# Performance work log

Hardware: AMD Instinct MI355X
Metric: run time of the kernel (lower is better)

The kernel has to match this reference:

```python
import jax, jax.numpy as jnp
import numpy as np

NUM_EXPERTS = 16
TOP_K = 2
HIDDEN = 2048
INTER = 1408
TOKENS = 4096


def setup_inputs() -> dict:
    key = jax.random.key(0)
    k0, k1, k2, k3, k4 = jax.random.split(key, 5)
    scale = 0.02
    return {
        "hidden_states": jax.random.normal(k0, (TOKENS, HIDDEN), jnp.float32),
        "router_logits": jax.random.normal(k1, (TOKENS, NUM_EXPERTS), jnp.float32),
        # SwiGLU expert weights, stacked over the expert dim.
        "w_gate": jax.random.normal(k2, (NUM_EXPERTS, HIDDEN, INTER), jnp.float32) * scale,
        "w_up": jax.random.normal(k3, (NUM_EXPERTS, HIDDEN, INTER), jnp.float32) * scale,
        "w_down": jax.random.normal(k4, (NUM_EXPERTS, INTER, HIDDEN), jnp.float32) * scale,
    }


def reference(hidden_states, router_logits, w_gate, w_up, w_down):
    # Routing (router_use_softmax=False branch): topk on raw logits,
    # then softmax over the selected top-k logits.
    topk_weights, topk_ids = jax.lax.top_k(router_logits, TOP_K)  # [T,K]
    topk_weights = jax.nn.softmax(topk_weights, axis=-1)

    T = hidden_states.shape[0]
    # Dense combine matrix [T, E]: weight of expert e for token t (0 if not selected).
    combine = jnp.zeros((T, NUM_EXPERTS), hidden_states.dtype)
    combine = combine.at[jnp.arange(T)[:, None], topk_ids].add(topk_weights)

    # Expert SwiGLU FFNs, computed densely over all tokens per expert and
    # masked/weighted by the combine matrix (same math as gather->FFN->scatter).
    g = jnp.einsum("th,ehi->eti", hidden_states, w_gate)  # [E,T,I]
    u = jnp.einsum("th,ehi->eti", hidden_states, w_up)    # [E,T,I]
    a = jax.nn.silu(g) * u                                  # [E,T,I]
    y = jnp.einsum("eti,eih->eth", a, w_down)             # [E,T,H]

    # Weighted scatter-combine: sum_e combine[t,e] * y[e,t,:]
    return jnp.einsum("eth,te->th", y, combine)            # [T,H]
```

## Files before the change

kernel.cpp:

```cpp
#include <hip/hip_runtime.h>
#include <hip/hip_bf16.h>
#include <cstdint>

#define NTOK 4096
#define NEXP 16
#define HID 2048
#define INTER 1408
#define BK 32
#define LDA 40
#define MAXTILES 80

typedef __attribute__((ext_vector_type(8))) short bf16x8;
typedef __attribute__((ext_vector_type(4))) float f32x4;


__device__ inline unsigned pack_bf16(float lo, float hi) {
  unsigned a = __builtin_bit_cast(unsigned, lo) + 0x8000u;
  unsigned b = __builtin_bit_cast(unsigned, hi) + 0x8000u;
  return __builtin_amdgcn_perm(b, a, 0x07060302u);
}

__global__ void k_router(const float* __restrict__ logits, int* __restrict__ topk_id,
                         float* __restrict__ topk_w, int* __restrict__ counts) {
  int t = blockIdx.x * blockDim.x + threadIdx.x;
  if (t >= NTOK) return;
  const float* l = logits + (size_t)t * NEXP;
  float b0 = -1e30f, b1 = -1e30f; int i0 = 0, i1 = 0;
#pragma unroll
  for (int i = 0; i < NEXP; i++) {
    float v = l[i];
    if (v > b0) { b1 = b0; i1 = i0; b0 = v; i0 = i; }
    else if (v > b1) { b1 = v; i1 = i; }
  }
  float e = __expf(b1 - b0);
  float inv = 1.f / (1.f + e);
  topk_id[t * 2] = i0; topk_id[t * 2 + 1] = i1;
  topk_w[t * 2] = inv; topk_w[t * 2 + 1] = e * inv;
  atomicAdd(&counts[i0], 1);
  atomicAdd(&counts[i1], 1);
}

__global__ void k_build(int* __restrict__ ws_i) {
  if (threadIdx.x == 0) {
    int off = 0, nt = 0;
    for (int e = 0; e < NEXP; e++) {
      int c = ws_i[e];
      ws_i[32 + e] = off;
      int tiles = (c + 127) >> 7;
      for (int mt = 0; mt < tiles; mt++) { ws_i[64 + nt] = e; ws_i[144 + nt] = mt; nt++; }
      off += c;
    }
    ws_i[48] = nt;
  }
}

__global__ void k_scatter(const int* __restrict__ topk_id, const float* __restrict__ topk_w,
                          int* __restrict__ ws_i, int* __restrict__ list_tok,
                          float* __restrict__ list_w) {
  int t = blockIdx.x * blockDim.x + threadIdx.x;
  if (t >= NTOK) return;
#pragma unroll
  for (int k = 0; k < 2; k++) {
    int e = topk_id[t * 2 + k];
    int slot = ws_i[32 + e] + atomicAdd(&ws_i[16 + e], 1);
    list_tok[slot] = t;
    list_w[slot] = topk_w[t * 2 + k];
  }
}

__global__ __launch_bounds__(256, 2) void k_gateup(
    const float* __restrict__ hidden, const float* __restrict__ w_gate,
    const float* __restrict__ w_up, const int* __restrict__ ws_i,
    const int* __restrict__ list_tok, __hip_bfloat16* __restrict__ act) {
  __shared__ unsigned short sA[128 * LDA];
  __shared__ unsigned short sBg[64 * LDA];
  __shared__ unsigned short sBu[64 * LDA];
  __shared__ int sTok[128];

  int tileId = blockIdx.y;
  if (tileId >= ws_i[48]) return;
  int e = ws_i[64 + tileId];
  int mt = ws_i[144 + tileId];
  int c = ws_i[e];
  int offE = ws_i[32 + e];
  int m0 = mt * 128;
  int n0 = blockIdx.x * 64;
  int tid = threadIdx.x;

  if (tid < 128) {
    int r = m0 + tid;
    int rr = r < c ? r : c - 1;
    sTok[tid] = list_tok[offE + rr];
  }
  __syncthreads();

  const float* wg = w_gate + (size_t)e * HID * INTER + n0;
  const float* wu = w_up + (size_t)e * HID * INTER + n0;

  int lane = tid & 63;
  int wave = tid >> 6;
  int wm = wave & 1, wn = wave >> 1;

  f32x4 accG[4][2], accU[4][2];
#pragma unroll
  for (int i = 0; i < 4; i++)
#pragma unroll
    for (int j = 0; j < 2; j++) { accG[i][j] = (f32x4)(0.f); accU[i][j] = (f32x4)(0.f); }

  int ar = tid >> 1;
  int ah = (tid & 1) * 16;
  const float* aSrc = hidden + (size_t)sTok[ar] * HID + ah;

  int bn = tid & 63;
  int bkg = tid >> 6;
  const float* bgSrc = wg + bn + (size_t)(bkg * 8) * INTER;
  const float* buSrc = wu + bn + (size_t)(bkg * 8) * INTER;

  int kq = (lane >> 4) * 8;
  int ml = lane & 15;

  for (int k0 = 0; k0 < HID; k0 += BK) {
    const float4* ap = (const float4*)(aSrc + k0);
    float4 a0 = ap[0], a1 = ap[1], a2 = ap[2], a3 = ap[3];
    float g[8], u[8];
    const float* bg = bgSrc + (size_t)k0 * INTER;
    const float* bu = buSrc + (size_t)k0 * INTER;
#pragma unroll
    for (int j = 0; j < 8; j++) { g[j] = bg[(size_t)j * INTER]; u[j] = bu[(size_t)j * INTER]; }

    __syncthreads();
    {
      uint4 w0 = make_uint4(pack_bf16(a0.x, a0.y), pack_bf16(a0.z, a0.w),
                            pack_bf16(a1.x, a1.y), pack_bf16(a1.z, a1.w));
      uint4 w1 = make_uint4(pack_bf16(a2.x, a2.y), pack_bf16(a2.z, a2.w),
                            pack_bf16(a3.x, a3.y), pack_bf16(a3.z, a3.w));
      *(uint4*)&sA[ar * LDA + ah] = w0;
      *(uint4*)&sA[ar * LDA + ah + 8] = w1;
      *(uint4*)&sBg[bn * LDA + bkg * 8] = make_uint4(
          pack_bf16(g[0], g[1]), pack_bf16(g[2], g[3]),
          pack_bf16(g[4], g[5]), pack_bf16(g[6], g[7]));
      *(uint4*)&sBu[bn * LDA + bkg * 8] = make_uint4(
          pack_bf16(u[0], u[1]), pack_bf16(u[2], u[3]),
          pack_bf16(u[4], u[5]), pack_bf16(u[6], u[7]));
    }
    __syncthreads();

    bf16x8 af[4], bgf[2], buf2[2];
#pragma unroll
    for (int ni = 0; ni < 2; ni++) {
      bgf[ni] = *(const bf16x8*)&sBg[(wn * 32 + ni * 16 + ml) * LDA + kq];
      buf2[ni] = *(const bf16x8*)&sBu[(wn * 32 + ni * 16 + ml) * LDA + kq];
    }
#pragma unroll
    for (int mi = 0; mi < 4; mi++)
      af[mi] = *(const bf16x8*)&sA[(wm * 64 + mi * 16 + ml) * LDA + kq];
#pragma unroll
    for (int mi = 0; mi < 4; mi++)
#pragma unroll
      for (int ni = 0; ni < 2; ni++) {
        accG[mi][ni] = __builtin_amdgcn_mfma_f32_16x16x32_bf16(af[mi], bgf[ni], accG[mi][ni], 0, 0, 0);
        accU[mi][ni] = __builtin_amdgcn_mfma_f32_16x16x32_bf16(af[mi], buf2[ni], accU[mi][ni], 0, 0, 0);
      }
  }

  int rq = (lane >> 4) * 4;
#pragma unroll
  for (int mi = 0; mi < 4; mi++)
#pragma unroll
    for (int r = 0; r < 4; r++) {
      int mrow = wm * 64 + mi * 16 + rq + r;
      int mglob = m0 + mrow;
      if (mglob < c) {
        size_t arow = (size_t)(offE + mglob);
#pragma unroll
        for (int ni = 0; ni < 2; ni++) {
          float gv = accG[mi][ni][r], uv = accU[mi][ni][r];
          float av = gv / (1.f + __expf(-gv)) * uv;
          int ncol = n0 + wn * 32 + ni * 16 + ml;
          act[arow * INTER + ncol] = __float2bfloat16(av);
        }
      }
    }
}

__global__ __launch_bounds__(256, 2) void k_down(
    const __hip_bfloat16* __restrict__ act, const float* __restrict__ w_down,
    const int* __restrict__ ws_i, const int* __restrict__ list_tok,
    const float* __restrict__ list_w, float* __restrict__ out) {
  __shared__ unsigned short sA[128 * LDA];
  __shared__ unsigned short sB[128 * LDA];
  __shared__ int sTok[128];
  __shared__ float sW[128];

  int tileId = blockIdx.y;
  if (tileId >= ws_i[48]) return;
  int e = ws_i[64 + tileId];
  int mt = ws_i[144 + tileId];
  int c = ws_i[e];
  int offE = ws_i[32 + e];
  int m0 = mt * 128;
  int n0 = blockIdx.x * 128;
  int tid = threadIdx.x;

  if (tid < 128) {
    int r = m0 + tid;
    int rr = r < c ? r : c - 1;
    sTok[tid] = list_tok[offE + rr];
    sW[tid] = list_w[offE + rr];
  }
  __syncthreads();

  int lane = tid & 63;
  int wave = tid >> 6;
  int wm = wave & 1, wn = wave >> 1;
  f32x4 acc[4][4];
#pragma unroll
  for (int i = 0; i < 4; i++)
#pragma unroll
    for (int j = 0; j < 4; j++) acc[i][j] = (f32x4)(0.f);

  int ar = tid >> 1;
  int ah = (tid & 1) * 16;
  const __hip_bfloat16* aRow;
  {
    int r = m0 + ar;
    int rr = r < c ? r : c - 1;
    aRow = act + (size_t)(offE + rr) * INTER + ah;
  }
  int bn = tid & 127;
  int bkg2 = tid >> 7;
  const float* bSrc = w_down + (size_t)e * INTER * HID + n0 + bn;

  int kq = (lane >> 4) * 8;
  int ml = lane & 15;

  for (int k0 = 0; k0 < INTER; k0 += BK) {
    const uint4* ap = (const uint4*)(aRow + k0);
    uint4 av0 = ap[0], av1 = ap[1];
    float b[2][8];
#pragma unroll
    for (int tsk = 0; tsk < 2; tsk++) {
      const float* bp = bSrc + (size_t)(k0 + (bkg2 * 2 + tsk) * 8) * HID;
#pragma unroll
      for (int j = 0; j < 8; j++) b[tsk][j] = bp[(size_t)j * HID];
    }

    __syncthreads();
    *(uint4*)&sA[ar * LDA + ah] = av0;
    *(uint4*)&sA[ar * LDA + ah + 8] = av1;
#pragma unroll
    for (int tsk = 0; tsk < 2; tsk++) {
      int kg = bkg2 * 2 + tsk;
      *(uint4*)&sB[bn * LDA + kg * 8] = make_uint4(
          pack_bf16(b[tsk][0], b[tsk][1]), pack_bf16(b[tsk][2], b[tsk][3]),
          pack_bf16(b[tsk][4], b[tsk][5]), pack_bf16(b[tsk][6], b[tsk][7]));
    }
    __syncthreads();

    bf16x8 af[4], bf[4];
#pragma unroll
    for (int mi = 0; mi < 4; mi++)
      af[mi] = *(const bf16x8*)&sA[(wm * 64 + mi * 16 + ml) * LDA + kq];
#pragma unroll
    for (int ni = 0; ni < 4; ni++)
      bf[ni] = *(const bf16x8*)&sB[(wn * 64 + ni * 16 + ml) * LDA + kq];
#pragma unroll
    for (int mi = 0; mi < 4; mi++)
#pragma unroll
      for (int ni = 0; ni < 4; ni++)
        acc[mi][ni] = __builtin_amdgcn_mfma_f32_16x16x32_bf16(af[mi], bf[ni], acc[mi][ni], 0, 0, 0);
  }

  int rq = (lane >> 4) * 4;
#pragma unroll
  for (int mi = 0; mi < 4; mi++)
#pragma unroll
    for (int r = 0; r < 4; r++) {
      int mrow = wm * 64 + mi * 16 + rq + r;
      if (m0 + mrow < c) {
        int t = sTok[mrow];
        float w = sW[mrow];
        float* op = out + (size_t)t * HID + n0 + wn * 64 + ml;
#pragma unroll
        for (int ni = 0; ni < 4; ni++)
          atomicAdd(op + ni * 16, w * acc[mi][ni][r]);
      }
    }
}

extern "C" void kernel_launch(void* const* d_in, const int* in_sizes, int n_in,
                              void* d_out, int out_size, void* d_ws, size_t ws_size,
                              hipStream_t stream) {
  const float* hidden = (const float*)d_in[0];
  const float* logits = (const float*)d_in[1];
  const float* w_gate = (const float*)d_in[2];
  const float* w_up = (const float*)d_in[3];
  const float* w_down = (const float*)d_in[4];
  float* out = (float*)d_out;

  int* ws_i = (int*)d_ws;
  int* topk_id = ws_i + 256;
  float* topk_w = (float*)(ws_i + 8448);
  int* list_tok = ws_i + 16640;
  float* list_w = (float*)(ws_i + 24832);
  __hip_bfloat16* act = (__hip_bfloat16*)((char*)d_ws + 33024 * 4);

  hipMemsetAsync(d_ws, 0, 256 * 4, stream);
  hipMemsetAsync(d_out, 0, (size_t)out_size * sizeof(float), stream);

  k_router<<<NTOK / 256, 256, 0, stream>>>(logits, topk_id, topk_w, ws_i);
  k_build<<<1, 64, 0, stream>>>(ws_i);
  k_scatter<<<NTOK / 256, 256, 0, stream>>>(topk_id, topk_w, ws_i, list_tok, list_w);
  k_gateup<<<dim3(INTER / 64, MAXTILES), 256, 0, stream>>>(hidden, w_gate, w_up, ws_i, list_tok, act);
  k_down<<<dim3(HID / 128, MAXTILES), 256, 0, stream>>>(act, w_down, ws_i, list_tok, list_w, out);
}
```

Before: 904.4 us.

## Pre-gather bf16 activations, prefetch tiles, and replace atomic scatter with combine kernel

Result: faster. 849.4 us (-6.1%).

```diff
diff --git a/kernel.cpp b/kernel.cpp
--- a/kernel.cpp
+++ b/kernel.cpp
@@ -56,7 +56,7 @@
 
 __global__ void k_scatter(const int* __restrict__ topk_id, const float* __restrict__ topk_w,
                           int* __restrict__ ws_i, int* __restrict__ list_tok,
-                          float* __restrict__ list_w) {
+                          float* __restrict__ list_w, int* __restrict__ slot_of) {
   int t = blockIdx.x * blockDim.x + threadIdx.x;
   if (t >= NTOK) return;
 #pragma unroll
@@ -65,17 +65,29 @@
     int slot = ws_i[32 + e] + atomicAdd(&ws_i[16 + e], 1);
     list_tok[slot] = t;
     list_w[slot] = topk_w[t * 2 + k];
-  }
-}
-
-__global__ __launch_bounds__(256, 2) void k_gateup(
-    const float* __restrict__ hidden, const float* __restrict__ w_gate,
+    slot_of[t * 2 + k] = slot;
+  }
+}
+
+__global__ __launch_bounds__(256) void k_gather(const float* __restrict__ hidden,
+                                                const int* __restrict__ list_tok,
+                                                unsigned short* __restrict__ Ab) {
+  int s = blockIdx.x, tx = threadIdx.x;
+  int t = list_tok[s];
+  const float4* src = (const float4*)(hidden + (size_t)t * HID) + tx * 2;
+  float4 a = src[0], b = src[1];
+  uint4 w = make_uint4(pack_bf16(a.x, a.y), pack_bf16(a.z, a.w),
+                       pack_bf16(b.x, b.y), pack_bf16(b.z, b.w));
+  ((uint4*)(Ab + (size_t)s * HID))[tx] = w;
+}
+
+__global__ __launch_bounds__(256, 4) void k_gateup(
+    const unsigned short* __restrict__ Ab, const float* __restrict__ w_gate,
     const float* __restrict__ w_up, const int* __restrict__ ws_i,
-    const int* __restrict__ list_tok, __hip_bfloat16* __restrict__ act) {
+    __hip_bfloat16* __restrict__ act) {
   __shared__ unsigned short sA[128 * LDA];
   __shared__ unsigned short sBg[64 * LDA];
   __shared__ unsigned short sBu[64 * LDA];
-  __shared__ int sTok[128];
 
   int tileId = blockIdx.y;
   if (tileId >= ws_i[48]) return;
@@ -87,63 +99,57 @@
   int n0 = blockIdx.x * 64;
   int tid = threadIdx.x;
 
-  if (tid < 128) {
-    int r = m0 + tid;
-    int rr = r < c ? r : c - 1;
-    sTok[tid] = list_tok[offE + rr];
-  }
-  __syncthreads();
-
-  const float* wg = w_gate + (size_t)e * HID * INTER + n0;
-  const float* wu = w_up + (size_t)e * HID * INTER + n0;
-
   int lane = tid & 63;
   int wave = tid >> 6;
   int wm = wave & 1, wn = wave >> 1;
 
-  f32x4 accG[4][2], accU[4][2];
-#pragma unroll
-  for (int i = 0; i < 4; i++)
-#pragma unroll
-    for (int j = 0; j < 2; j++) { accG[i][j] = (f32x4)(0.f); accU[i][j] = (f32x4)(0.f); }
-
   int ar = tid >> 1;
   int ah = (tid & 1) * 16;
-  const float* aSrc = hidden + (size_t)sTok[ar] * HID + ah;
+  int rA = m0 + ar; int rrA = rA < c ? rA : c - 1;
+  const unsigned short* aSrc = Ab + (size_t)(offE + rrA) * HID + ah;
 
   int bn = tid & 63;
   int bkg = tid >> 6;
-  const float* bgSrc = wg + bn + (size_t)(bkg * 8) * INTER;
-  const float* buSrc = wu + bn + (size_t)(bkg * 8) * INTER;
+  const float* bgSrc = w_gate + (size_t)e * HID * INTER + n0 + bn + (size_t)(bkg * 8) * INTER;
+  const float* buSrc = w_up   + (size_t)e * HID * INTER + n0 + bn + (size_t)(bkg * 8) * INTER;
+
+  f32x4 accG[4][2], accU[4][2];
+#pragma unroll
+  for (int i = 0; i < 4; i++)
+#pragma unroll
+    for (int j = 0; j < 2; j++) { accG[i][j] = (f32x4)(0.f); accU[i][j] = (f32x4)(0.f); }
 
   int kq = (lane >> 4) * 8;
   int ml = lane & 15;
 
+  uint4 a0r, a1r; float g[8], u[8];
+  {
+    const uint4* ap = (const uint4*)aSrc;
+    a0r = ap[0]; a1r = ap[1];
+#pragma unroll
+    for (int j = 0; j < 8; j++) { g[j] = bgSrc[(size_t)j * INTER]; u[j] = buSrc[(size_t)j * INTER]; }
+  }
+
   for (int k0 = 0; k0 < HID; k0 += BK) {
-    const float4* ap = (const float4*)(aSrc + k0);
-    float4 a0 = ap[0], a1 = ap[1], a2 = ap[2], a3 = ap[3];
-    float g[8], u[8];
-    const float* bg = bgSrc + (size_t)k0 * INTER;
-    const float* bu = buSrc + (size_t)k0 * INTER;
-#pragma unroll
-    for (int j = 0; j < 8; j++) { g[j] = bg[(size_t)j * INTER]; u[j] = bu[(size_t)j * INTER]; }
-
     __syncthreads();
-    {
-      uint4 w0 = make_uint4(pack_bf16(a0.x, a0.y), pack_bf16(a0.z, a0.w),
-                            pack_bf16(a1.x, a1.y), pack_bf16(a1.z, a1.w));
-      uint4 w1 = make_uint4(pack_bf16(a2.x, a2.y), pack_bf16(a2.z, a2.w),
-                            pack_bf16(a3.x, a3.y), pack_bf16(a3.z, a3.w));
-      *(uint4*)&sA[ar * LDA + ah] = w0;
-      *(uint4*)&sA[ar * LDA + ah + 8] = w1;
-      *(uint4*)&sBg[bn * LDA + bkg * 8] = make_uint4(
-          pack_bf16(g[0], g[1]), pack_bf16(g[2], g[3]),
-          pack_bf16(g[4], g[5]), pack_bf16(g[6], g[7]));
-      *(uint4*)&sBu[bn * LDA + bkg * 8] = make_uint4(
-          pack_bf16(u[0], u[1]), pack_bf16(u[2], u[3]),
-          pack_bf16(u[4], u[5]), pack_bf16(u[6], u[7]));
-    }
+    *(uint4*)&sA[ar * LDA + ah] = a0r;
+    *(uint4*)&sA[ar * LDA + ah + 8] = a1r;
+    *(uint4*)&sBg[bn * LDA + bkg * 8] = make_uint4(
+        pack_bf16(g[0], g[1]), pack_bf16(g[2], g[3]),
+        pack_bf16(g[4], g[5]), pack_bf16(g[6], g[7]));
+    *(uint4*)&sBu[bn * LDA + bkg * 8] = make_uint4(
+        pack_bf16(u[0], u[1]), pack_bf16(u[2], u[3]),
+        pack_bf16(u[4], u[5]), pack_bf16(u[6], u[7]));
     __syncthreads();
+
+    if (k0 + BK < HID) {
+      const uint4* ap = (const uint4*)(aSrc + k0 + BK);
+      a0r = ap[0]; a1r = ap[1];
+      const float* bg = bgSrc + (size_t)(k0 + BK) * INTER;
+      const float* bu = buSrc + (size_t)(k0 + BK) * INTER;
+#pragma unroll
+      for (int j = 0; j < 8; j++) { g[j] = bg[(size_t)j * INTER]; u[j] = bu[(size_t)j * INTER]; }
+    }
 
     bf16x8 af[4], bgf[2], buf2[2];
 #pragma unroll
@@ -183,13 +189,12 @@
     }
 }
 
-__global__ __launch_bounds__(256, 2) void k_down(
+__global__ __launch_bounds__(256, 4) void k_down(
     const __hip_bfloat16* __restrict__ act, const float* __restrict__ w_down,
-    const int* __restrict__ ws_i, const int* __restrict__ list_tok,
-    const float* __restrict__ list_w, float* __restrict__ out) {
+    const int* __restrict__ ws_i, const float* __restrict__ list_w,
+    unsigned short* __restrict__ y) {
   __shared__ unsigned short sA[128 * LDA];
-  __shared__ unsigned short sB[128 * LDA];
-  __shared__ int sTok[128];
+  __shared__ unsigned short sB[64 * LDA];
   __shared__ float sW[128];
 
   int tileId = blockIdx.y;
@@ -199,75 +204,72 @@
   int c = ws_i[e];
   int offE = ws_i[32 + e];
   int m0 = mt * 128;
-  int n0 = blockIdx.x * 128;
+  int n0 = blockIdx.x * 64;
   int tid = threadIdx.x;
 
   if (tid < 128) {
     int r = m0 + tid;
     int rr = r < c ? r : c - 1;
-    sTok[tid] = list_tok[offE + rr];
     sW[tid] = list_w[offE + rr];
   }
-  __syncthreads();
 
   int lane = tid & 63;
   int wave = tid >> 6;
   int wm = wave & 1, wn = wave >> 1;
-  f32x4 acc[4][4];
+  f32x4 acc[4][2];
 #pragma unroll
   for (int i = 0; i < 4; i++)
 #pragma unroll
-    for (int j = 0; j < 4; j++) acc[i][j] = (f32x4)(0.f);
+    for (int j = 0; j < 2; j++) acc[i][j] = (f32x4)(0.f);
 
   int ar = tid >> 1;
   int ah = (tid & 1) * 16;
-  const __hip_bfloat16* aRow;
-  {
-    int r = m0 + ar;
-    int rr = r < c ? r : c - 1;
-    aRow = act + (size_t)(offE + rr) * INTER + ah;
-  }
-  int bn = tid & 127;
-  int bkg2 = tid >> 7;
-  const float* bSrc = w_down + (size_t)e * INTER * HID + n0 + bn;
+  int rA = m0 + ar; int rrA = rA < c ? rA : c - 1;
+  const unsigned short* aSrc = (const unsigned short*)act + (size_t)(offE + rrA) * INTER + ah;
+
+  int bn = tid & 63;
+  int bkg = tid >> 6;
+  const float* bSrc = w_down + (size_t)e * INTER * HID + (size_t)(bkg * 8) * HID + n0 + bn;
 
   int kq = (lane >> 4) * 8;
   int ml = lane & 15;
 
+  uint4 a0r, a1r; float b[8];
+  {
+    const uint4* ap = (const uint4*)aSrc;
+    a0r = ap[0]; a1r = ap[1];
+#pragma unroll
+    for (int j = 0; j < 8; j++) b[j] = bSrc[(size_t)j * HID];
+  }
+
   for (int k0 = 0; k0 < INTER; k0 += BK) {
-    const uint4* ap = (const uint4*)(aRow + k0);
-    uint4 av0 = ap[0], av1 = ap[1];
-    float b[2][8];
-#pragma unroll
-    for (int tsk = 0; tsk < 2; tsk++) {
-      const float* bp = bSrc + (size_t)(k0 + (bkg2 * 2 + tsk) * 8) * HID;
-#pragma unroll
-      for (int j = 0; j < 8; j++) b[tsk][j] = bp[(size_t)j * HID];
-    }
-
     __syncthreads();
-    *(uint4*)&sA[ar * LDA + ah] = av0;
-    *(uint4*)&sA[ar * LDA + ah + 8] = av1;
-#pragma unroll
-    for (int tsk = 0; tsk < 2; tsk++) {
-      int kg = bkg2 * 2 + tsk;
-      *(uint4*)&sB[bn * LDA + kg * 8] = make_uint4(
-          pack_bf16(b[tsk][0], b[tsk][1]), pack_bf16(b[tsk][2], b[tsk][3]),
-          pack_bf16(b[tsk][4], b[tsk][5]), pack_bf16(b[tsk][6], b[tsk][7]));
-    }
+    *(uint4*)&sA[ar * LDA + ah] = a0r;
+    *(uint4*)&sA[ar * LDA + ah + 8] = a1r;
+    *(uint4*)&sB[bn * LDA + bkg * 8] = make_uint4(
+        pack_bf16(b[0], b[1]), pack_bf16(b[2], b[3]),
+        pack_bf16(b[4], b[5]), pack_bf16(b[6], b[7]));
     __syncthreads();
 
-    bf16x8 af[4], bf[4];
+    if (k0 + BK < INTER) {
+      const uint4* ap = (const uint4*)(aSrc + k0 + BK);
+      a0r = ap[0]; a1r = ap[1];
+      const float* bp = bSrc + (size_t)(k0 + BK) * HID;
+#pragma unroll
+      for (int j = 0; j < 8; j++) b[j] = bp[(size_t)j * HID];
+    }
+
+    bf16x8 af[4], bf[2];
+#pragma unroll
+    for (int ni = 0; ni < 2; ni++)
+      bf[ni] = *(const bf16x8*)&sB[(wn * 32 + ni * 16 + ml) * LDA + kq];
 #pragma unroll
     for (int mi = 0; mi < 4; mi++)
       af[mi] = *(const bf16x8*)&sA[(wm * 64 + mi * 16 + ml) * LDA + kq];
 #pragma unroll
-    for (int ni = 0; ni < 4; ni++)
-      bf[ni] = *(const bf16x8*)&sB[(wn * 64 + ni * 16 + ml) * LDA + kq];
-#pragma unroll
     for (int mi = 0; mi < 4; mi++)
 #pragma unroll
-      for (int ni = 0; ni < 4; ni++)
+      for (int ni = 0; ni < 2; ni++)
         acc[mi][ni] = __builtin_amdgcn_mfma_f32_16x16x32_bf16(af[mi], bf[ni], acc[mi][ni], 0, 0, 0);
   }
 
@@ -278,14 +280,39 @@
     for (int r = 0; r < 4; r++) {
       int mrow = wm * 64 + mi * 16 + rq + r;
       if (m0 + mrow < c) {
-        int t = sTok[mrow];
         float w = sW[mrow];
-        float* op = out + (size_t)t * HID + n0 + wn * 64 + ml;
-#pragma unroll
-        for (int ni = 0; ni < 4; ni++)
-          atomicAdd(op + ni * 16, w * acc[mi][ni][r]);
+        size_t yrow = (size_t)(offE + m0 + mrow);
+#pragma unroll
+        for (int ni = 0; ni < 2; ni++) {
+          int ncol = n0 + wn * 32 + ni * 16 + ml;
+          float v = w * acc[mi][ni][r];
+          y[yrow * HID + ncol] = (unsigned short)(pack_bf16(v, 0.f) & 0xffffu);
+        }
       }
     }
+}
+
+__global__ __launch_bounds__(256) void k_combine(const unsigned short* __restrict__ y,
+                                                 const int* __restrict__ slot_of,
+                                                 float* __restrict__ out) {
+  int t = blockIdx.x, tx = threadIdx.x;
+  size_t s0 = (size_t)slot_of[t * 2], s1 = (size_t)slot_of[t * 2 + 1];
+  uint4 v0 = ((const uint4*)(y + s0 * HID))[tx];
+  uint4 v1 = ((const uint4*)(y + s1 * HID))[tx];
+  float r[8];
+  unsigned p0[4] = {v0.x, v0.y, v0.z, v0.w};
+  unsigned p1[4] = {v1.x, v1.y, v1.z, v1.w};
+#pragma unroll
+  for (int i = 0; i < 4; i++) {
+    float lo0 = __builtin_bit_cast(float, p0[i] << 16);
+    float hi0 = __builtin_bit_cast(float, p0[i] & 0xffff0000u);
+    float lo1 = __builtin_bit_cast(float, p1[i] << 16);
+    float hi1 = __builtin_bit_cast(float, p1[i] & 0xffff0000u);
+    r[i * 2] = lo0 + lo1; r[i * 2 + 1] = hi0 + hi1;
+  }
+  float4* op = (float4*)(out + (size_t)t * HID) + tx * 2;
+  op[0] = make_float4(r[0], r[1], r[2], r[3]);
+  op[1] = make_float4(r[4], r[5], r[6], r[7]);
 }
 
 extern "C" void kernel_launch(void* const* d_in, const int* in_sizes, int n_in,
@@ -303,14 +330,17 @@
   float* topk_w = (float*)(ws_i + 8448);
   int* list_tok = ws_i + 16640;
   float* list_w = (float*)(ws_i + 24832);
-  __hip_bfloat16* act = (__hip_bfloat16*)((char*)d_ws + 33024 * 4);
+  int* slot_of = ws_i + 33024;
+  __hip_bfloat16* act = (__hip_bfloat16*)((char*)d_ws + 262144);
+  unsigned short* AbY = (unsigned short*)((char*)d_ws + 23330816);
 
   hipMemsetAsync(d_ws, 0, 256 * 4, stream);
-  hipMemsetAsync(d_out, 0, (size_t)out_size * sizeof(float), stream);
 
   k_router<<<NTOK / 256, 256, 0, stream>>>(logits, topk_id, topk_w, ws_i);
   k_build<<<1, 64, 0, stream>>>(ws_i);
-  k_scatter<<<NTOK / 256, 256, 0, stream>>>(topk_id, topk_w, ws_i, list_tok, list_w);
-  k_gateup<<<dim3(INTER / 64, MAXTILES), 256, 0, stream>>>(hidden, w_gate, w_up, ws_i, list_tok, act);
-  k_down<<<dim3(HID / 128, MAXTILES), 256, 0, stream>>>(act, w_down, ws_i, list_tok, list_w, out);
-}
+  k_scatter<<<NTOK / 256, 256, 0, stream>>>(topk_id, topk_w, ws_i, list_tok, list_w, slot_of);
+  k_gather<<<NTOK * 2, 256, 0, stream>>>(hidden, list_tok, AbY);
+  k_gateup<<<dim3(INTER / 64, MAXTILES), 256, 0, stream>>>(AbY, w_gate, w_up, ws_i, act);
+  k_down<<<dim3(HID / 64, MAXTILES), 256, 0, stream>>>(act, w_down, ws_i, list_w, AbY);
+  k_combine<<<NTOK, 256, 0, stream>>>(AbY, slot_of, out);
+}
```
